# Kernel optimization log

Measured on AMD Instinct MI355X. Metric: run time of the kernel, lower is better.

The kernel has to match this reference:

```python
import jax, jax.numpy as jnp
import numpy as np


def setup_inputs() -> dict:
    key = jax.random.key(0)
    k1, k2 = jax.random.split(key)
    B, Tc, Tq, D = 8, 2048, 1024, 1024
    similarity = jax.random.normal(k1, (B, Tc, Tq), dtype=jnp.float32)
    qencode = jax.random.normal(k2, (B, Tq, D), dtype=jnp.float32)
    return {"similarity": similarity, "qencode": qencode}


def reference(similarity, qencode):
    # softmax over query axis, then weighted sum of query encodings:
    # equivalent to softmax(similarity, -1) @ qencode, avoiding the
    # [B, Tc, Tq, D] broadcasted intermediate of the original TF code.
    attn = jax.nn.softmax(similarity, axis=-1)          # [B, Tc, Tq]
    c2q = jnp.einsum("bcq,bqd->bcd", attn, qencode)     # [B, Tc, D]
    return c2q
```

## Files before the change

kernel.cpp:

```cpp
#include <hip/hip_runtime.h>
#include <hip/hip_bf16.h>
#include <stdint.h>

#define BATCH 8
#define TC 2048
#define TQ 1024
#define DD 1024

typedef __attribute__((ext_vector_type(8))) __bf16 bf16x8;
typedef __attribute__((ext_vector_type(4))) float f32x4;

__device__ __forceinline__ ushort f2bf(float f) {
    uint32_t u = __float_as_uint(f);
    uint32_t r = (u + 0x7fffu + ((u >> 16) & 1u)) >> 16;
    return (ushort)r;
}

__global__ __launch_bounds__(256) void softmax_rows(const float* __restrict__ sim,
                                                    ushort* __restrict__ attn) {
    const int wid = threadIdx.x >> 6;
    const int lane = threadIdx.x & 63;
    const int row = blockIdx.x * 4 + wid;
    const float4* src = (const float4*)(sim + (size_t)row * TQ);

    float4 x[4];
    #pragma unroll
    for (int j = 0; j < 4; j++) x[j] = src[lane + 64 * j];

    float m = -INFINITY;
    #pragma unroll
    for (int j = 0; j < 4; j++)
        m = fmaxf(m, fmaxf(fmaxf(x[j].x, x[j].y), fmaxf(x[j].z, x[j].w)));
    #pragma unroll
    for (int o = 32; o >= 1; o >>= 1) m = fmaxf(m, __shfl_xor(m, o));

    const float L2E = 1.4426950408889634f;
    float e[4][4];
    float s = 0.f;
    #pragma unroll
    for (int j = 0; j < 4; j++) {
        e[j][0] = exp2f((x[j].x - m) * L2E);
        e[j][1] = exp2f((x[j].y - m) * L2E);
        e[j][2] = exp2f((x[j].z - m) * L2E);
        e[j][3] = exp2f((x[j].w - m) * L2E);
        s += (e[j][0] + e[j][1]) + (e[j][2] + e[j][3]);
    }
    #pragma unroll
    for (int o = 32; o >= 1; o >>= 1) s += __shfl_xor(s, o);
    const float inv = 1.0f / s;

    ushort4* dst = (ushort4*)(attn + (size_t)row * TQ);
    #pragma unroll
    for (int j = 0; j < 4; j++) {
        ushort4 o4;
        o4.x = f2bf(e[j][0] * inv);
        o4.y = f2bf(e[j][1] * inv);
        o4.z = f2bf(e[j][2] * inv);
        o4.w = f2bf(e[j][3] * inv);
        dst[lane + 64 * j] = o4;
    }
}

__global__ __launch_bounds__(256) void transpose_cast(const float* __restrict__ q,
                                                      ushort* __restrict__ qt) {
    __shared__ float tile[64][65];
    const int b = blockIdx.z;
    const int q0 = blockIdx.y * 64;
    const int d0 = blockIdx.x * 64;
    const int t = threadIdx.x;
    const int r = t >> 4;
    const int c = (t & 15) * 4;

    #pragma unroll
    for (int it = 0; it < 4; it++) {
        float4 v = *(const float4*)(q + ((size_t)b * TQ + q0 + r + it * 16) * DD + d0 + c);
        tile[r + it * 16][c + 0] = v.x;
        tile[r + it * 16][c + 1] = v.y;
        tile[r + it * 16][c + 2] = v.z;
        tile[r + it * 16][c + 3] = v.w;
    }
    __syncthreads();

    #pragma unroll
    for (int it = 0; it < 4; it++) {
        const int d = (t >> 4) + it * 16;
        const int qq = (t & 15) * 4;
        ushort4 o4;
        o4.x = f2bf(tile[qq + 0][d]);
        o4.y = f2bf(tile[qq + 1][d]);
        o4.z = f2bf(tile[qq + 2][d]);
        o4.w = f2bf(tile[qq + 3][d]);
        *(ushort4*)(qt + ((size_t)b * DD + d0 + d) * TQ + q0 + qq) = o4;
    }
}

__global__ __launch_bounds__(256, 2) void gemm_bf16(const ushort* __restrict__ A,
                                                    const ushort* __restrict__ Bt,
                                                    float* __restrict__ C) {
    __shared__ __align__(16) ushort As[128 * 32];
    __shared__ __align__(16) ushort Bs[128 * 32];

    const int flat = blockIdx.x;
    const int b = flat >> 7;
    const int rem = flat & 127;
    const int group = rem >> 5;
    const int mi_t = group * 4 + (rem & 3);
    const int ni_t = (rem >> 2) & 7;
    const int tm0 = mi_t * 128;
    const int tn0 = ni_t * 128;

    const ushort* Ab = A + (size_t)b * TC * TQ;
    const ushort* Bb = Bt + (size_t)b * DD * TQ;
    float* Cb = C + (size_t)b * TC * DD;

    const int t = threadIdx.x;
    const int w = t >> 6, lane = t & 63;
    const int quad = lane >> 4, l16 = lane & 15;
    const int wm = (w >> 1) * 64, wn = (w & 1) * 64;

    f32x4 acc[4][4];
    #pragma unroll
    for (int i = 0; i < 4; i++)
        #pragma unroll
        for (int j = 0; j < 4; j++) acc[i][j] = (f32x4){0.f, 0.f, 0.f, 0.f};

    const int srow = w * 16 + (lane >> 2);
    const int sk = (lane & 3) * 8;

    for (int kk = 0; kk < TQ; kk += 32) {
        #pragma unroll
        for (int j = 0; j < 2; j++) {
            const ushort* ga = Ab + (size_t)(tm0 + j * 64 + srow) * TQ + kk + sk;
            const ushort* gb = Bb + (size_t)(tn0 + j * 64 + srow) * TQ + kk + sk;
            char* la = (char*)As + j * 4096 + w * 1024;
            char* lb = (char*)Bs + j * 4096 + w * 1024;
            __builtin_amdgcn_global_load_lds(
                (const __attribute__((address_space(1))) void*)ga,
                (__attribute__((address_space(3))) void*)la, 16, 0, 0);
            __builtin_amdgcn_global_load_lds(
                (const __attribute__((address_space(1))) void*)gb,
                (__attribute__((address_space(3))) void*)lb, 16, 0, 0);
        }
        __syncthreads();

        bf16x8 af[4], bfr[4];
        #pragma unroll
        for (int mi = 0; mi < 4; mi++)
            af[mi] = *(const bf16x8*)&As[(wm + mi * 16 + l16) * 32 + quad * 8];
        #pragma unroll
        for (int ni = 0; ni < 4; ni++)
            bfr[ni] = *(const bf16x8*)&Bs[(wn + ni * 16 + l16) * 32 + quad * 8];

        #pragma unroll
        for (int mi = 0; mi < 4; mi++)
            #pragma unroll
            for (int ni = 0; ni < 4; ni++)
                acc[mi][ni] = __builtin_amdgcn_mfma_f32_16x16x32_bf16(
                    af[mi], bfr[ni], acc[mi][ni], 0, 0, 0);
        __syncthreads();
    }

    #pragma unroll
    for (int mi = 0; mi < 4; mi++) {
        const int r0 = tm0 + wm + mi * 16 + quad * 4;
        #pragma unroll
        for (int ni = 0; ni < 4; ni++) {
            const int c = tn0 + wn + ni * 16 + l16;
            f32x4 v = acc[mi][ni];
            #pragma unroll
            for (int r = 0; r < 4; r++) Cb[(size_t)(r0 + r) * DD + c] = v[r];
        }
    }
}

extern "C" void kernel_launch(void* const* d_in, const int* in_sizes, int n_in,
                              void* d_out, int out_size, void* d_ws, size_t ws_size,
                              hipStream_t stream) {
    const float* sim = (const float*)d_in[0];
    const float* qen = (const float*)d_in[1];
    float* out = (float*)d_out;

    ushort* attn = (ushort*)d_ws;
    ushort* qt = (ushort*)d_ws + (size_t)BATCH * TC * TQ;

    softmax_rows<<<BATCH * TC / 4, 256, 0, stream>>>(sim, attn);
    transpose_cast<<<dim3(DD / 64, TQ / 64, BATCH), 256, 0, stream>>>(qen, qt);
    gemm_bf16<<<BATCH * (TC / 128) * (DD / 128), 256, 0, stream>>>(attn, qt, out);
}
```

Measured before the change: 186.2 us.

## Merge prep kernels and switch GEMM to 256x128 tiles with 32x32 MFMA and LDS swizzle

Softmax and the transpose-cast now run as one merged launch, with a block-index split deciding which job each block does. The GEMM tile grows from 128x128 to 256x128, and each wave computes 128x64 using the 32x32x16 bf16 MFMA instead of 16x16x32. An XOR swizzle on LDS chunk columns is meant to reduce bank conflicts on fragment reads. Together these aim to raise arithmetic intensity per LDS byte and cut one launch. The cost is more accumulator registers and a grid of only 512 blocks, which may underfill the 256 CUs at 2 blocks per CU.

```diff
diff --git a/kernel.cpp b/kernel.cpp
--- a/kernel.cpp
+++ b/kernel.cpp
@@ -8,7 +8,7 @@
 #define DD 1024
 
 typedef __attribute__((ext_vector_type(8))) __bf16 bf16x8;
-typedef __attribute__((ext_vector_type(4))) float f32x4;
+typedef __attribute__((ext_vector_type(16))) float f32x16;
 
 __device__ __forceinline__ ushort f2bf(float f) {
     uint32_t u = __float_as_uint(f);
@@ -16,98 +16,98 @@
     return (ushort)r;
 }
 
-__global__ __launch_bounds__(256) void softmax_rows(const float* __restrict__ sim,
-                                                    ushort* __restrict__ attn) {
-    const int wid = threadIdx.x >> 6;
-    const int lane = threadIdx.x & 63;
-    const int row = blockIdx.x * 4 + wid;
-    const float4* src = (const float4*)(sim + (size_t)row * TQ);
-
-    float4 x[4];
-    #pragma unroll
-    for (int j = 0; j < 4; j++) x[j] = src[lane + 64 * j];
-
-    float m = -INFINITY;
-    #pragma unroll
-    for (int j = 0; j < 4; j++)
-        m = fmaxf(m, fmaxf(fmaxf(x[j].x, x[j].y), fmaxf(x[j].z, x[j].w)));
-    #pragma unroll
-    for (int o = 32; o >= 1; o >>= 1) m = fmaxf(m, __shfl_xor(m, o));
-
-    const float L2E = 1.4426950408889634f;
-    float e[4][4];
-    float s = 0.f;
-    #pragma unroll
-    for (int j = 0; j < 4; j++) {
-        e[j][0] = exp2f((x[j].x - m) * L2E);
-        e[j][1] = exp2f((x[j].y - m) * L2E);
-        e[j][2] = exp2f((x[j].z - m) * L2E);
-        e[j][3] = exp2f((x[j].w - m) * L2E);
-        s += (e[j][0] + e[j][1]) + (e[j][2] + e[j][3]);
-    }
-    #pragma unroll
-    for (int o = 32; o >= 1; o >>= 1) s += __shfl_xor(s, o);
-    const float inv = 1.0f / s;
-
-    ushort4* dst = (ushort4*)(attn + (size_t)row * TQ);
-    #pragma unroll
-    for (int j = 0; j < 4; j++) {
-        ushort4 o4;
-        o4.x = f2bf(e[j][0] * inv);
-        o4.y = f2bf(e[j][1] * inv);
-        o4.z = f2bf(e[j][2] * inv);
-        o4.w = f2bf(e[j][3] * inv);
-        dst[lane + 64 * j] = o4;
-    }
-}
-
-__global__ __launch_bounds__(256) void transpose_cast(const float* __restrict__ q,
-                                                      ushort* __restrict__ qt) {
+__global__ __launch_bounds__(256) void prep(const float* __restrict__ sim,
+                                            const float* __restrict__ qen,
+                                            ushort* __restrict__ attn,
+                                            ushort* __restrict__ qt) {
     __shared__ float tile[64][65];
-    const int b = blockIdx.z;
-    const int q0 = blockIdx.y * 64;
-    const int d0 = blockIdx.x * 64;
     const int t = threadIdx.x;
-    const int r = t >> 4;
-    const int c = (t & 15) * 4;
-
-    #pragma unroll
-    for (int it = 0; it < 4; it++) {
-        float4 v = *(const float4*)(q + ((size_t)b * TQ + q0 + r + it * 16) * DD + d0 + c);
-        tile[r + it * 16][c + 0] = v.x;
-        tile[r + it * 16][c + 1] = v.y;
-        tile[r + it * 16][c + 2] = v.z;
-        tile[r + it * 16][c + 3] = v.w;
-    }
-    __syncthreads();
-
-    #pragma unroll
-    for (int it = 0; it < 4; it++) {
-        const int d = (t >> 4) + it * 16;
-        const int qq = (t & 15) * 4;
-        ushort4 o4;
-        o4.x = f2bf(tile[qq + 0][d]);
-        o4.y = f2bf(tile[qq + 1][d]);
-        o4.z = f2bf(tile[qq + 2][d]);
-        o4.w = f2bf(tile[qq + 3][d]);
-        *(ushort4*)(qt + ((size_t)b * DD + d0 + d) * TQ + q0 + qq) = o4;
+    if (blockIdx.x < 4096) {
+        const int wid = t >> 6;
+        const int lane = t & 63;
+        const int row = blockIdx.x * 4 + wid;
+        const float4* src = (const float4*)(sim + (size_t)row * TQ);
+
+        float4 x[4];
+        #pragma unroll
+        for (int j = 0; j < 4; j++) x[j] = src[lane + 64 * j];
+
+        float m = -INFINITY;
+        #pragma unroll
+        for (int j = 0; j < 4; j++)
+            m = fmaxf(m, fmaxf(fmaxf(x[j].x, x[j].y), fmaxf(x[j].z, x[j].w)));
+        #pragma unroll
+        for (int o = 32; o >= 1; o >>= 1) m = fmaxf(m, __shfl_xor(m, o));
+
+        const float L2E = 1.4426950408889634f;
+        float e[4][4];
+        float s = 0.f;
+        #pragma unroll
+        for (int j = 0; j < 4; j++) {
+            e[j][0] = exp2f((x[j].x - m) * L2E);
+            e[j][1] = exp2f((x[j].y - m) * L2E);
+            e[j][2] = exp2f((x[j].z - m) * L2E);
+            e[j][3] = exp2f((x[j].w - m) * L2E);
+            s += (e[j][0] + e[j][1]) + (e[j][2] + e[j][3]);
+        }
+        #pragma unroll
+        for (int o = 32; o >= 1; o >>= 1) s += __shfl_xor(s, o);
+        const float inv = 1.0f / s;
+
+        ushort4* dst = (ushort4*)(attn + (size_t)row * TQ);
+        #pragma unroll
+        for (int j = 0; j < 4; j++) {
+            ushort4 o4;
+            o4.x = f2bf(e[j][0] * inv);
+            o4.y = f2bf(e[j][1] * inv);
+            o4.z = f2bf(e[j][2] * inv);
+            o4.w = f2bf(e[j][3] * inv);
+            dst[lane + 64 * j] = o4;
+        }
+    } else {
+        const int bid = blockIdx.x - 4096;
+        const int b = bid >> 8;
+        const int rem = bid & 255;
+        const int q0 = (rem >> 4) * 64;
+        const int d0 = (rem & 15) * 64;
+        const int r = t >> 4;
+        const int c = (t & 15) * 4;
+
+        #pragma unroll
+        for (int it = 0; it < 4; it++) {
+            float4 v = *(const float4*)(qen + ((size_t)b * TQ + q0 + r + it * 16) * DD + d0 + c);
+            tile[r + it * 16][c + 0] = v.x;
+            tile[r + it * 16][c + 1] = v.y;
+            tile[r + it * 16][c + 2] = v.z;
+            tile[r + it * 16][c + 3] = v.w;
+        }
+        __syncthreads();
+
+        #pragma unroll
+        for (int it = 0; it < 4; it++) {
+            const int d = (t >> 4) + it * 16;
+            const int qq = (t & 15) * 4;
+            ushort4 o4;
+            o4.x = f2bf(tile[qq + 0][d]);
+            o4.y = f2bf(tile[qq + 1][d]);
+            o4.z = f2bf(tile[qq + 2][d]);
+            o4.w = f2bf(tile[qq + 3][d]);
+            *(ushort4*)(qt + ((size_t)b * DD + d0 + d) * TQ + q0 + qq) = o4;
+        }
     }
 }
 
 __global__ __launch_bounds__(256, 2) void gemm_bf16(const ushort* __restrict__ A,
                                                     const ushort* __restrict__ Bt,
                                                     float* __restrict__ C) {
-    __shared__ __align__(16) ushort As[128 * 32];
+    __shared__ __align__(16) ushort As[256 * 32];
     __shared__ __align__(16) ushort Bs[128 * 32];
 
     const int flat = blockIdx.x;
-    const int b = flat >> 7;
-    const int rem = flat & 127;
-    const int group = rem >> 5;
-    const int mi_t = group * 4 + (rem & 3);
-    const int ni_t = (rem >> 2) & 7;
-    const int tm0 = mi_t * 128;
-    const int tn0 = ni_t * 128;
+    const int b = flat >> 6;
+    const int rem = flat & 63;
+    const int tm0 = (rem & 7) * 256;
+    const int tn0 = (rem >> 3) * 128;
 
     const ushort* Ab = A + (size_t)b * TC * TQ;
     const ushort* Bb = Bt + (size_t)b * DD * TQ;
@@ -115,60 +115,78 @@
 
     const int t = threadIdx.x;
     const int w = t >> 6, lane = t & 63;
-    const int quad = lane >> 4, l16 = lane & 15;
-    const int wm = (w >> 1) * 64, wn = (w & 1) * 64;
-
-    f32x4 acc[4][4];
+    const int row32 = lane & 31, half = lane >> 5;
+    const int wm = (w >> 1) * 128, wn = (w & 1) * 64;
+
+    f32x16 acc[4][2];
     #pragma unroll
     for (int i = 0; i < 4; i++)
         #pragma unroll
-        for (int j = 0; j < 4; j++) acc[i][j] = (f32x4){0.f, 0.f, 0.f, 0.f};
-
-    const int srow = w * 16 + (lane >> 2);
-    const int sk = (lane & 3) * 8;
+        for (int j = 0; j < 2; j++)
+            #pragma unroll
+            for (int r = 0; r < 16; r++) acc[i][j][r] = 0.f;
 
     for (int kk = 0; kk < TQ; kk += 32) {
         #pragma unroll
-        for (int j = 0; j < 2; j++) {
-            const ushort* ga = Ab + (size_t)(tm0 + j * 64 + srow) * TQ + kk + sk;
-            const ushort* gb = Bb + (size_t)(tn0 + j * 64 + srow) * TQ + kk + sk;
-            char* la = (char*)As + j * 4096 + w * 1024;
-            char* lb = (char*)Bs + j * 4096 + w * 1024;
+        for (int i = 0; i < 4; i++) {
+            const int p = i * 256 + w * 64 + lane;
+            const int r = p >> 2, x = p & 3;
+            const int c = x ^ (r & 3);
+            const ushort* ga = Ab + (size_t)(tm0 + r) * TQ + kk + c * 8;
             __builtin_amdgcn_global_load_lds(
                 (const __attribute__((address_space(1))) void*)ga,
-                (__attribute__((address_space(3))) void*)la, 16, 0, 0);
+                (__attribute__((address_space(3))) void*)((char*)As + i * 4096 + w * 1024),
+                16, 0, 0);
+        }
+        #pragma unroll
+        for (int i = 0; i < 2; i++) {
+            const int p = i * 256 + w * 64 + lane;
+            const int r = p >> 2, x = p & 3;
+            const int c = x ^ (r & 3);
+            const ushort* gb = Bb + (size_t)(tn0 + r) * TQ + kk + c * 8;
             __builtin_amdgcn_global_load_lds(
                 (const __attribute__((address_space(1))) void*)gb,
-                (__attribute__((address_space(3))) void*)lb, 16, 0, 0);
+                (__attribute__((address_space(3))) void*)((char*)Bs + i * 4096 + w * 1024),
+                16, 0, 0);
         }
         __syncthreads();
 
-        bf16x8 af[4], bfr[4];
-        #pragma unroll
-        for (int mi = 0; mi < 4; mi++)
-            af[mi] = *(const bf16x8*)&As[(wm + mi * 16 + l16) * 32 + quad * 8];
-        #pragma unroll
-        for (int ni = 0; ni < 4; ni++)
-            bfr[ni] = *(const bf16x8*)&Bs[(wn + ni * 16 + l16) * 32 + quad * 8];
-
-        #pragma unroll
-        for (int mi = 0; mi < 4; mi++)
-            #pragma unroll
-            for (int ni = 0; ni < 4; ni++)
-                acc[mi][ni] = __builtin_amdgcn_mfma_f32_16x16x32_bf16(
-                    af[mi], bfr[ni], acc[mi][ni], 0, 0, 0);
+        #pragma unroll
+        for (int s = 0; s < 2; s++) {
+            const int c = s * 2 + half;
+            bf16x8 af[4], bfr[2];
+            #pragma unroll
+            for (int mb = 0; mb < 4; mb++) {
+                const int r = wm + mb * 32 + row32;
+                af[mb] = *(const bf16x8*)&As[r * 32 + (c ^ (r & 3)) * 8];
+            }
+            #pragma unroll
+            for (int nb = 0; nb < 2; nb++) {
+                const int r = wn + nb * 32 + row32;
+                bfr[nb] = *(const bf16x8*)&Bs[r * 32 + (c ^ (r & 3)) * 8];
+            }
+            #pragma unroll
+            for (int mb = 0; mb < 4; mb++)
+                #pragma unroll
+                for (int nb = 0; nb < 2; nb++)
+                    acc[mb][nb] = __builtin_amdgcn_mfma_f32_32x32x16_bf16(
+                        af[mb], bfr[nb], acc[mb][nb], 0, 0, 0);
+        }
         __syncthreads();
     }
 
     #pragma unroll
-    for (int mi = 0; mi < 4; mi++) {
-        const int r0 = tm0 + wm + mi * 16 + quad * 4;
-        #pragma unroll
-        for (int ni = 0; ni < 4; ni++) {
-            const int c = tn0 + wn + ni * 16 + l16;
-            f32x4 v = acc[mi][ni];
-            #pragma unroll
-            for (int r = 0; r < 4; r++) Cb[(size_t)(r0 + r) * DD + c] = v[r];
+    for (int mb = 0; mb < 4; mb++) {
+        #pragma unroll
+        for (int nb = 0; nb < 2; nb++) {
+            const int colg = tn0 + wn + nb * 32 + row32;
+            const int rbase = tm0 + wm + mb * 32 + 4 * half;
+            f32x16 v = acc[mb][nb];
+            #pragma unroll
+            for (int reg = 0; reg < 16; reg++) {
+                const int rowg = rbase + (reg & 3) + 8 * (reg >> 2);
+                Cb[(size_t)rowg * DD + colg] = v[reg];
+            }
         }
     }
 }
@@ -183,7 +201,6 @@
     ushort* attn = (ushort*)d_ws;
     ushort* qt = (ushort*)d_ws + (size_t)BATCH * TC * TQ;
 
-    softmax_rows<<<BATCH * TC / 4, 256, 0, stream>>>(sim, attn);
-    transpose_cast<<<dim3(DD / 64, TQ / 64, BATCH), 256, 0, stream>>>(qen, qt);
-    gemm_bf16<<<BATCH * (TC / 128) * (DD / 128), 256, 0, stream>>>(attn, qt, out);
-}
+    prep<<<4096 + 2048, 256, 0, stream>>>(sim, qen, attn, qt);
+    gemm_bf16<<<BATCH * 8 * 8, 256, 0, stream>>>(attn, qt, out);
+}
```

Measured after the change: 187.5 us. No clear change (+0.7%).
